# Kernel tuning notes

Hardware: AMD Instinct MI355X
Metric: run time of the kernel (lower is better)

The kernel has to match this reference:

```python
import jax, jax.numpy as jnp
import numpy as np

BATCH = 16384
NFEAT = 16          # 12 non-rainfall + 4 rainfall (indices 12..15)
NNON, NRAIN = 12, 4
NC = 1000           # n_clusters
DM = 64             # d_model
DI = 128            # d_inner = expand * d_model
DS = 16             # d_state
DC = 4              # d_conv
DR = 4              # dt_rank = ceil(d_model / 16)
NL = 4              # n_layers
EPS = 1e-5


def _silu(v):
    return v * jax.nn.sigmoid(v)


def _layernorm(v, g, b):
    m = jnp.mean(v, -1, keepdims=True)
    s = jnp.mean(jnp.square(v - m), -1, keepdims=True)
    return (v - m) * jax.lax.rsqrt(s + EPS) * g + b


def _mamba(x, ipw, cw, cb, xpw, dtw, dtb, alog, dskip, opw):
    # x: [B, L, DM]
    Bsz, L, _ = x.shape
    xz = x @ ipw                                # [B, L, 2*DI]
    xc, z = jnp.split(xz, 2, axis=-1)
    # causal depthwise conv1d (kernel DC, left pad DC-1)
    xp = jnp.pad(xc, ((0, 0), (DC - 1, 0), (0, 0)))
    xc = sum(xp[:, k:k + L, :] * cw[:, k] for k in range(DC)) + cb
    xc = _silu(xc)
    proj = xc @ xpw                             # [B, L, DR + 2*DS]
    dt = jax.nn.softplus(proj[..., :DR] @ dtw + dtb)   # [B, L, DI]
    Bm = proj[..., DR:DR + DS]                  # [B, L, DS]
    Cm = proj[..., DR + DS:]                    # [B, L, DS]
    A = -jnp.exp(alog)                          # [DI, DS]
    dA = jnp.exp(dt[..., None] * A)             # [B, L, DI, DS]
    dBx = dt[..., None] * Bm[:, :, None, :] * xc[..., None]

    def step(h, ab):
        a, b = ab
        h = a * h + b
        return h, h

    _, hs = jax.lax.scan(step, jnp.zeros((Bsz, DI, DS), x.dtype),
                         (jnp.swapaxes(dA, 0, 1), jnp.swapaxes(dBx, 0, 1)))
    hs = jnp.swapaxes(hs, 0, 1)                 # [B, L, DI, DS]
    y = jnp.einsum('blds,bls->bld', hs, Cm) + dskip * xc
    y = y * _silu(z)
    return y @ opw                              # [B, L, DM]


def _branch(feat, w_in, b_in, ipw, cw, cb, xpw, dtw, dtb, alog, dskip, opw, ln_g, ln_b):
    x = (feat @ w_in + b_in)[:, None, :]        # [B, 1, DM]
    for l in range(NL):
        x = x + _layernorm(
            _mamba(x, ipw[l], cw[l], cb[l], xpw[l], dtw[l], dtb[l], alog[l], dskip[l], opw[l]),
            ln_g[l], ln_b[l])
    return jnp.mean(x, axis=1)                  # [B, DM]


def _forward(x, w_nr, b_nr, w_r, b_r, w_in_nr, b_in_nr, w_in_r, b_in_r,
             ipw, cw, cb, xpw, dtw, dtb, alog, dskip, opw, ln_g, ln_b,
             head_w1, head_b1, head_w2, head_b2):
    nr = x[:, :NNON] @ w_nr + b_nr              # non-rainfall cluster proj [B, NC]
    r = x[:, NNON:] @ w_r + b_r                 # rainfall cluster proj [B, NC]
    # NOTE: mamba layers + norms are SHARED between both branches (as in the torch module)
    o_nr = _branch(nr, w_in_nr, b_in_nr, ipw, cw, cb, xpw, dtw, dtb, alog, dskip, opw, ln_g, ln_b)
    o_r = _branch(r, w_in_r, b_in_r, ipw, cw, cb, xpw, dtw, dtb, alog, dskip, opw, ln_g, ln_b)
    h = jnp.concatenate([o_nr, o_r], axis=-1)   # [B, 2*DM]
    h = jax.nn.relu(h @ head_w1 + head_b1)
    return (h @ head_w2 + head_b2)[:, 0]        # [B]


def setup_inputs() -> dict:
    key = jax.random.key(0)
    kit = iter(jax.random.split(key, 32))

    def rn(shape, s=0.05):
        return jax.random.normal(next(kit), shape, jnp.float32) * s

    return {
        'x': jax.random.normal(next(kit), (BATCH, NFEAT), jnp.float32),
        'w_nr': rn((NNON, NC)), 'b_nr': rn((NC,)),
        'w_r': rn((NRAIN, NC)), 'b_r': rn((NC,)),
        'w_in_nr': rn((NC, DM)), 'b_in_nr': rn((DM,)),
        'w_in_r': rn((NC, DM)), 'b_in_r': rn((DM,)),
        'ipw': rn((NL, DM, 2 * DI)),
        'cw': rn((NL, DI, DC)), 'cb': rn((NL, DI)),
        'xpw': rn((NL, DI, DR + 2 * DS)),
        'dtw': rn((NL, DR, DI)), 'dtb': rn((NL, DI)),
        'alog': jnp.log(jnp.broadcast_to(jnp.arange(1, DS + 1, dtype=jnp.float32), (NL, DI, DS))),
        'dskip': jnp.ones((NL, DI), jnp.float32),
        'opw': rn((NL, DI, DM)),
        'ln_g': jnp.ones((NL, DM), jnp.float32),
        'ln_b': jnp.zeros((NL, DM), jnp.float32),
        'head_w1': rn((2 * DM, 32)), 'head_b1': rn((32,)),
        'head_w2': rn((32, 1)), 'head_b2': rn((1,)),
    }


def reference(x, w_nr, b_nr, w_r, b_r, w_in_nr, b_in_nr, w_in_r, b_in_r,
              ipw, cw, cb, xpw, dtw, dtb, alog, dskip, opw, ln_g, ln_b,
              head_w1, head_b1, head_w2, head_b2):
    return _forward(x, w_nr, b_nr, w_r, b_r, w_in_nr, b_in_nr, w_in_r, b_in_r,
                    ipw, cw, cb, xpw, dtw, dtb, alog, dskip, opw, ln_g, ln_b,
                    head_w1, head_b1, head_w2, head_b2)
```

## Files before the change

### kernel.cpp

```cpp
#include <hip/hip_runtime.h>
#include <hip/hip_bf16.h>
#include <math.h>

typedef unsigned short u16;
typedef unsigned int u32;
typedef __attribute__((ext_vector_type(8))) short bf8v;
typedef __attribute__((ext_vector_type(4))) float f32x4;

#define BR   32
#define LR   64
#define NLAY 4

#define U_IPH 4096
#define U_IPL (U_IPH + 65536)
#define U_XPH (U_IPL + 65536)
#define U_XPL (U_XPH + 24576)
#define U_OPH (U_XPL + 24576)
#define U_OPL (U_OPH + 32768)

__device__ __forceinline__ float b2f(u16 u) {
  u32 x = ((u32)u) << 16; return __uint_as_float(x);
}
__device__ __forceinline__ u16 f2b(float f) {
  __hip_bfloat16 b = __float2bfloat16(f);
  return __builtin_bit_cast(u16, b);
}
__device__ __forceinline__ void splitbf(float v, u16& h, u16& l) {
  h = f2b(v);
  l = f2b(v - b2f(h));
}
__device__ __forceinline__ float siluf(float v) { return v / (1.f + __expf(-v)); }
__device__ __forceinline__ float softplusf(float v) {
  return fmaxf(v, 0.f) + __logf(1.f + __expf(-fabsf(v)));
}
__device__ __forceinline__ int sxIdx(int r, int c) {
  return r * 64 + ((((c >> 3) ^ r) & 7) << 3) + (c & 7);
}
__device__ __forceinline__ int szIdx(int r, int c) {
  int ch = c >> 3;
  int chs = (ch & 8) | ((ch ^ r) & 7);
  return r * 128 + chs * 8 + (c & 7);
}

#define MFMA16(A, B, C) __builtin_amdgcn_mfma_f32_16x16x32_bf16(A, B, C, 0, 0, 0)

extern "C" __global__ __launch_bounds__(256)
void prep_all_kernel(const float* __restrict__ w_nr, const float* __restrict__ b_nr,
                     const float* __restrict__ w_r,  const float* __restrict__ b_r,
                     const float* __restrict__ win_nr, const float* __restrict__ bin_nr,
                     const float* __restrict__ win_r,  const float* __restrict__ bin_r,
                     const float* __restrict__ ipw, const float* __restrict__ xpw,
                     const float* __restrict__ opw,
                     float* __restrict__ wsf, u16* __restrict__ wsu) {
  __shared__ float snr[1000];
  __shared__ float sr_[1000];
  const int bid = blockIdx.x, tid = threadIdx.x;
  if (bid < 64) {
    const int j = bid;
    for (int k = tid; k < 1000; k += 256) {
      snr[k] = win_nr[(size_t)k * 64 + j];
      sr_[k] = win_r [(size_t)k * 64 + j];
    }
    __syncthreads();
    const int grp = tid >> 4;
    const int ks  = tid & 15;
    const int k0 = ks * 63, k1 = (k0 + 63 < 1000) ? k0 + 63 : 1000;
    for (int o = grp; o < 18; o += 16) {
      float acc = 0.f;
      if (o < 12) {
        const float* s = w_nr + (size_t)o * 1000;
        for (int k = k0; k < k1; ++k) acc = fmaf(s[k], snr[k], acc);
      } else if (o == 12) {
        for (int k = k0; k < k1; ++k) acc = fmaf(b_nr[k], snr[k], acc);
      } else if (o < 17) {
        const float* s = w_r + (size_t)(o - 13) * 1000;
        for (int k = k0; k < k1; ++k) acc = fmaf(s[k], sr_[k], acc);
      } else {
        for (int k = k0; k < k1; ++k) acc = fmaf(b_r[k], sr_[k], acc);
      }
      for (int off = 1; off < 16; off <<= 1) acc += __shfl_xor(acc, off, 64);
      if (ks == 0) {
        if (o < 12)       wsf[o * 64 + j] = acc;
        else if (o == 12) wsf[768 + j]  = acc + bin_nr[j];
        else if (o < 17)  wsf[832 + (o - 13) * 64 + j] = acc;
        else              wsf[1088 + j] = acc + bin_r[j];
      }
    }
    return;
  }
  int gid = (bid - 64) * 256 + tid;
  float v; int dh, dl;
  if (gid < 65536) {
    int l = gid >> 14, rem = gid & 16383;
    int n = rem & 255, k = rem >> 8;
    v = ipw[(size_t)l * 16384 + k * 256 + n];
    int o = l * 16384 + n * 64 + k;
    dh = U_IPH + o; dl = U_IPL + o;
  } else if (gid < 65536 + 18432) {
    int e = gid - 65536;
    int l = e / 4608, r2 = e - l * 4608;
    int k = r2 / 36, n = r2 - k * 36;
    v = xpw[(size_t)l * 4608 + k * 36 + n];
    int o = l * 6144 + n * 128 + k;
    dh = U_XPH + o; dl = U_XPL + o;
  } else if (gid < 65536 + 18432 + 6144) {
    int e = gid - 83968;
    int l = e / 1536, r3 = e - l * 1536;
    int n = 36 + (r3 >> 7), k = r3 & 127;
    v = 0.f;
    int o = l * 6144 + n * 128 + k;
    dh = U_XPH + o; dl = U_XPL + o;
  } else {
    int e = gid - 90112;
    int l = e >> 13, rem = e & 8191;
    int n = rem & 63, k = rem >> 6;
    v = opw[(size_t)l * 8192 + k * 64 + n];
    int o = l * 8192 + n * 128 + k;
    dh = U_OPH + o; dl = U_OPL + o;
  }
  u16 h, lo; splitbf(v, h, lo);
  wsu[dh] = h; wsu[dl] = lo;
}

extern "C" __global__ __launch_bounds__(512, 3)
void mamba_main_kernel(const float* __restrict__ xin, const float* __restrict__ wsf,
                       const u16* __restrict__ wsu,
                       const float* __restrict__ cw, const float* __restrict__ cbi,
                       const float* __restrict__ dtw, const float* __restrict__ dtb,
                       const float* __restrict__ dskip,
                       const float* __restrict__ lng, const float* __restrict__ lnb,
                       const float* __restrict__ hw1, const float* __restrict__ hb1,
                       const float* __restrict__ hw2, const float* __restrict__ hb2,
                       float* __restrict__ outp)
{
  __shared__ __align__(16) u16 sxh[LR * 64], sxl[LR * 64];
  __shared__ __align__(16) u16 szh[LR * 128], szl[LR * 128];
  __shared__ __align__(16) u16 szb[LR * 128];
  __shared__ __align__(16) float sproj[LR * 48];
  __shared__ float spart[4][LR][2];
  __shared__ float sbc[LR];

  const int tid = threadIdx.x;
  const int wv = tid >> 6, lane = tid & 63;
  const int col16 = lane & 15, g = lane >> 4;
  const int r0 = blockIdx.x * BR;

  for (int idx = tid; idx < LR * 64; idx += 512) {
    int r = idx >> 6, c = idx & 63;
    const float* xr = xin + (size_t)(r0 + (r & 31)) * 16;
    float acc;
    if (r < 32) {
      acc = wsf[768 + c];
      #pragma unroll
      for (int i = 0; i < 12; ++i) acc = fmaf(xr[i], wsf[i * 64 + c], acc);
    } else {
      acc = wsf[1088 + c];
      #pragma unroll
      for (int i = 0; i < 4; ++i) acc = fmaf(xr[12 + i], wsf[832 + i * 64 + c], acc);
    }
    u16 h, lo; splitbf(acc, h, lo);
    int di = sxIdx(r, c); sxh[di] = h; sxl[di] = lo;
  }

  for (int l = 0; l < NLAY; ++l) {
    __syncthreads();
    {
      const u16* iph = wsu + U_IPH + l * 16384;
      const u16* ipl_ = wsu + U_IPL + l * 16384;
      const bool isZ = (wv >= 4);
      #pragma unroll 1
      for (int tt = 0; tt < 2; ++tt) {
        const int tile = 2 * wv + tt;
        const int n = tile * 16 + col16;
        bf8v Wh0 = *(const bf8v*)&iph[n * 64 + g * 8];
        bf8v Wl0 = *(const bf8v*)&ipl_[n * 64 + g * 8];
        bf8v Wh1 = *(const bf8v*)&iph[n * 64 + 32 + g * 8];
        bf8v Wl1 = *(const bf8v*)&ipl_[n * 64 + 32 + g * 8];
        float c3 = 0.f, cc = 0.f;
        int colx = (tile & 7) * 16 + col16;
        if (!isZ) {
          c3 = cw[(size_t)l * 512 + colx * 4 + 3];
          cc = cbi[(size_t)l * 128 + colx];
        }
        #pragma unroll 1
        for (int rt = 0; rt < 4; ++rt) {
          const int rowA = rt * 16 + col16;
          bf8v Ah0 = *(const bf8v*)&sxh[rowA * 64 + (((g ^ rowA) & 7) << 3)];
          bf8v Al0 = *(const bf8v*)&sxl[rowA * 64 + (((g ^ rowA) & 7) << 3)];
          bf8v Ah1 = *(const bf8v*)&sxh[rowA * 64 + ((((4 + g) ^ rowA) & 7) << 3)];
          bf8v Al1 = *(const bf8v*)&sxl[rowA * 64 + ((((4 + g) ^ rowA) & 7) << 3)];
          f32x4 acc = {0, 0, 0, 0};
          acc = MFMA16(Ah0, Wh0, acc);
          acc = MFMA16(Al0, Wh0, acc);
          acc = MFMA16(Ah0, Wl0, acc);
          acc = MFMA16(Ah1, Wh1, acc);
          acc = MFMA16(Al1, Wh1, acc);
          acc = MFMA16(Ah1, Wl1, acc);
          #pragma unroll
          for (int j = 0; j < 4; ++j) {
            int row = rt * 16 + g * 4 + j;
            if (!isZ) {
              float v = siluf(fmaf(acc[j], c3, cc));
              u16 h, lo; splitbf(v, h, lo);
              int di = szIdx(row, colx);
              szh[di] = h; szl[di] = lo;
            } else {
              szb[szIdx(row, colx)] = f2b(siluf(acc[j]));
            }
          }
        }
      }
    }
    __syncthreads();
    {
      const u16* xph = wsu + U_XPH + l * 6144;
      const u16* xpl = wsu + U_XPL + l * 6144;
      const int rt = wv & 3;
      const int rowA = rt * 16 + col16;
      const int ntasks = (wv < 4) ? 2 : 1;
      #pragma unroll 1
      for (int q = 0; q < ntasks; ++q) {
        const int nt = (wv < 4) ? q : 2;
        const int n2 = nt * 16 + col16;
        f32x4 C = {0, 0, 0, 0};
        #pragma unroll
        for (int ks = 0; ks < 4; ++ks) {
          int ch = ks * 4 + g;
          int ai = rowA * 128 + (((ch & 8) | ((ch ^ rowA) & 7)) << 3);
          bf8v Ah = *(const bf8v*)&szh[ai];
          bf8v Al = *(const bf8v*)&szl[ai];
          bf8v Wh = *(const bf8v*)&xph[n2 * 128 + ks * 32 + g * 8];
          bf8v Wl = *(const bf8v*)&xpl[n2 * 128 + ks * 32 + g * 8];
          C = MFMA16(Ah, Wh, C);
          C = MFMA16(Al, Wh, C);
          C = MFMA16(Ah, Wl, C);
        }
        #pragma unroll
        for (int j = 0; j < 4; ++j)
          sproj[(rt * 16 + g * 4 + j) * 48 + nt * 16 + col16] = C[j];
      }
    }
    __syncthreads();
    {
      int r = tid >> 3, s = tid & 7;
      float v = sproj[r * 48 + 4 + s] * sproj[r * 48 + 20 + s]
              + sproj[r * 48 + 12 + s] * sproj[r * 48 + 28 + s];
      v += __shfl_xor(v, 1); v += __shfl_xor(v, 2); v += __shfl_xor(v, 4);
      if (s == 0) sbc[r] = v;
    }
    __syncthreads();
    {
      const int rt = wv & 3;
      const int ctb = (wv >> 2) * 4;
      #pragma unroll 1
      for (int t = 0; t < 4; ++t) {
        int col = (ctb + t) * 16 + col16;
        float w0 = dtw[(size_t)l * 512 + col];
        float w1 = dtw[(size_t)l * 512 + 128 + col];
        float w2 = dtw[(size_t)l * 512 + 256 + col];
        float w3 = dtw[(size_t)l * 512 + 384 + col];
        float bb = dtb[(size_t)l * 128 + col];
        float ds = dskip[(size_t)l * 128 + col];
        #pragma unroll
        for (int j = 0; j < 4; ++j) {
          int r = rt * 16 + g * 4 + j;
          float4 pj = *(const float4*)&sproj[r * 48];
          float dtv = softplusf(fmaf(pj.w, w3, fmaf(pj.z, w2, fmaf(pj.y, w1, fmaf(pj.x, w0, bb)))));
          int di = szIdx(r, col);
          float xc = b2f(szh[di]) + b2f(szl[di]);
          float zv = b2f(szb[di]);
          float y = xc * fmaf(dtv, sbc[r], ds) * zv;
          u16 h, lo; splitbf(y, h, lo);
          szh[di] = h; szl[di] = lo;
        }
      }
    }
    __syncthreads();
    f32x4 O0 = {0,0,0,0}, O1 = {0,0,0,0};
    {
      const u16* oph = wsu + U_OPH + l * 8192;
      const u16* opl = wsu + U_OPL + l * 8192;
      const int nt = wv & 3, rtp = wv >> 2;
      const int n = nt * 16 + col16;
      #pragma unroll
      for (int ks = 0; ks < 4; ++ks) {
        bf8v Wh = *(const bf8v*)&oph[n * 128 + ks * 32 + g * 8];
        bf8v Wl = *(const bf8v*)&opl[n * 128 + ks * 32 + g * 8];
        int ch = ks * 4 + g;
        #pragma unroll
        for (int rr = 0; rr < 2; ++rr) {
          int rowA = (2 * rtp + rr) * 16 + col16;
          int ai = rowA * 128 + (((ch & 8) | ((ch ^ rowA) & 7)) << 3);
          bf8v Ah = *(const bf8v*)&szh[ai];
          bf8v Al = *(const bf8v*)&szl[ai];
          if (rr == 0) {
            O0 = MFMA16(Ah, Wh, O0); O0 = MFMA16(Al, Wh, O0); O0 = MFMA16(Ah, Wl, O0);
          } else {
            O1 = MFMA16(Ah, Wh, O1); O1 = MFMA16(Al, Wh, O1); O1 = MFMA16(Ah, Wl, O1);
          }
        }
      }
      #pragma unroll
      for (int rr = 0; rr < 2; ++rr) {
        #pragma unroll
        for (int j = 0; j < 4; ++j) {
          float o = (rr == 0) ? O0[j] : O1[j];
          float s1 = o, s2 = o * o;
          s1 += __shfl_xor(s1, 1); s2 += __shfl_xor(s2, 1);
          s1 += __shfl_xor(s1, 2); s2 += __shfl_xor(s2, 2);
          s1 += __shfl_xor(s1, 4); s2 += __shfl_xor(s2, 4);
          s1 += __shfl_xor(s1, 8); s2 += __shfl_xor(s2, 8);
          if (col16 == 0) {
            int row = (2 * rtp + rr) * 16 + g * 4 + j;
            spart[nt][row][0] = s1; spart[nt][row][1] = s2;
          }
        }
      }
    }
    __syncthreads();
    {
      const int nt = wv & 3, rtp = wv >> 2;
      int col = nt * 16 + col16;
      float gv = lng[(size_t)l * 64 + col], bv = lnb[(size_t)l * 64 + col];
      #pragma unroll
      for (int rr = 0; rr < 2; ++rr) {
        #pragma unroll
        for (int j = 0; j < 4; ++j) {
          int row = (2 * rtp + rr) * 16 + g * 4 + j;
          float s1 = spart[0][row][0] + spart[1][row][0] + spart[2][row][0] + spart[3][row][0];
          float s2 = spart[0][row][1] + spart[1][row][1] + spart[2][row][1] + spart[3][row][1];
          float m = s1 * (1.f / 64);
          float var = s2 * (1.f / 64) - m * m;
          float rstd = rsqrtf(var + 1e-5f);
          float o = (rr == 0) ? O0[j] : O1[j];
          float v = fmaf((o - m) * rstd, gv, bv);
          int di = sxIdx(row, col);
          float nv = b2f(sxh[di]) + b2f(sxl[di]) + v;
          u16 h, lo; splitbf(nv, h, lo);
          sxh[di] = h; sxl[di] = lo;
        }
      }
    }
  }
  __syncthreads();
  {
    int k = tid >> 2, n0 = (tid & 3) * 8;
    const float* src = hw1 + (size_t)k * 32 + n0;
    #pragma unroll
    for (int i = 0; i < 8; ++i) {
      u16 h, lo; splitbf(src[i], h, lo);
      int di = szIdx(n0 + i, k);
      szh[di] = h; szl[di] = lo;
    }
  }
  __syncthreads();
  if (wv < 4) {
    const int mt = wv & 1, nt = wv >> 1;
    const int m16 = mt * 16 + col16;
    const int nB = nt * 16 + col16;
    f32x4 H = {0, 0, 0, 0};
    #pragma unroll
    for (int ks = 0; ks < 4; ++ks) {
      int kg = ks * 32 + g * 8;
      int arow = m16 + ((kg >> 6) << 5);
      int ai = sxIdx(arow, kg & 63);
      bf8v Ah = *(const bf8v*)&sxh[ai];
      bf8v Al = *(const bf8v*)&sxl[ai];
      int bi = szIdx(nB, kg);
      bf8v Bh = *(const bf8v*)&szh[bi];
      bf8v Bl = *(const bf8v*)&szl[bi];
      H = MFMA16(Ah, Bh, H);
      H = MFMA16(Al, Bh, H);
      H = MFMA16(Ah, Bl, H);
    }
    float bias = hb1[nB];
    #pragma unroll
    for (int j = 0; j < 4; ++j) {
      int m = mt * 16 + g * 4 + j;
      sproj[m * 48 + nB] = fmaxf(H[j] + bias, 0.f);
    }
  }
  __syncthreads();
  if (tid < 256) {
    int m = tid >> 3, s = tid & 7;
    float acc = sproj[m * 48 + s] * hw2[s]
              + sproj[m * 48 + 8 + s] * hw2[8 + s]
              + sproj[m * 48 + 16 + s] * hw2[16 + s]
              + sproj[m * 48 + 24 + s] * hw2[24 + s];
    acc += __shfl_xor(acc, 1); acc += __shfl_xor(acc, 2); acc += __shfl_xor(acc, 4);
    if (s == 0) outp[r0 + m] = acc + hb2[0];
  }
}

extern "C" void kernel_launch(void* const* d_in, const int* in_sizes, int n_in,
                              void* d_out, int out_size, void* d_ws, size_t ws_size,
                              hipStream_t stream) {
  const float* x      = (const float*)d_in[0];
  const float* w_nr   = (const float*)d_in[1];
  const float* b_nr   = (const float*)d_in[2];
  const float* w_r    = (const float*)d_in[3];
  const float* b_r    = (const float*)d_in[4];
  const float* win_nr = (const float*)d_in[5];
  const float* bin_nr = (const float*)d_in[6];
  const float* win_r  = (const float*)d_in[7];
  const float* bin_r  = (const float*)d_in[8];
  const float* ipw    = (const float*)d_in[9];
  const float* cw     = (const float*)d_in[10];
  const float* cb     = (const float*)d_in[11];
  const float* xpw    = (const float*)d_in[12];
  const float* dtw    = (const float*)d_in[13];
  const float* dtb    = (const float*)d_in[14];
  const float* dskip  = (const float*)d_in[16];
  const float* opw    = (const float*)d_in[17];
  const float* lng    = (const float*)d_in[18];
  const float* lnb    = (const float*)d_in[19];
  const float* hw1    = (const float*)d_in[20];
  const float* hb1    = (const float*)d_in[21];
  const float* hw2    = (const float*)d_in[22];
  const float* hb2    = (const float*)d_in[23];
  float* wsf = (float*)d_ws;
  u16*   wsu = (u16*)d_ws;
  float* out = (float*)d_out;

  prep_all_kernel<<<544, 256, 0, stream>>>(w_nr, b_nr, w_r, b_r,
                                           win_nr, bin_nr, win_r, bin_r,
                                           ipw, xpw, opw, wsf, wsu);
  mamba_main_kernel<<<16384 / BR, 512, 0, stream>>>(x, wsf, wsu, cw, cb,
                                                    dtw, dtb, dskip, lng, lnb,
                                                    hw1, hb1, hw2, hb2, out);
}
```

Measured before the change: 225.2 us.

## Restructure weight-prep kernel with LDS-tiled transposes and vectorized bf16 split stores

Rewrites the prep kernel that folds the cluster projections and converts the Mamba weights to split bf16. The fold now uses one block per output row, reading win coalesced across lanes. The weight transposes stage tiles in padded shared memory and write the hi/lo parts as 16-byte vectors instead of scattered 2-byte stores. The grid shrinks from 544 to 42 blocks, so each block does more serial work and fewer CUs are used for a small prologue.

```diff
diff --git a/kernel.cpp b/kernel.cpp
--- a/kernel.cpp
+++ b/kernel.cpp
@@ -52,74 +52,110 @@
                      const float* __restrict__ ipw, const float* __restrict__ xpw,
                      const float* __restrict__ opw,
                      float* __restrict__ wsf, u16* __restrict__ wsu) {
-  __shared__ float snr[1000];
-  __shared__ float sr_[1000];
+  __shared__ float tileF[128 * 65];
   const int bid = blockIdx.x, tid = threadIdx.x;
-  if (bid < 64) {
-    const int j = bid;
-    for (int k = tid; k < 1000; k += 256) {
-      snr[k] = win_nr[(size_t)k * 64 + j];
-      sr_[k] = win_r [(size_t)k * 64 + j];
-    }
-    __syncthreads();
-    const int grp = tid >> 4;
-    const int ks  = tid & 15;
-    const int k0 = ks * 63, k1 = (k0 + 63 < 1000) ? k0 + 63 : 1000;
-    for (int o = grp; o < 18; o += 16) {
-      float acc = 0.f;
-      if (o < 12) {
-        const float* s = w_nr + (size_t)o * 1000;
-        for (int k = k0; k < k1; ++k) acc = fmaf(s[k], snr[k], acc);
-      } else if (o == 12) {
-        for (int k = k0; k < k1; ++k) acc = fmaf(b_nr[k], snr[k], acc);
-      } else if (o < 17) {
-        const float* s = w_r + (size_t)(o - 13) * 1000;
-        for (int k = k0; k < k1; ++k) acc = fmaf(s[k], sr_[k], acc);
-      } else {
-        for (int k = k0; k < k1; ++k) acc = fmaf(b_r[k], sr_[k], acc);
-      }
-      for (int off = 1; off < 16; off <<= 1) acc += __shfl_xor(acc, off, 64);
-      if (ks == 0) {
-        if (o < 12)       wsf[o * 64 + j] = acc;
-        else if (o == 12) wsf[768 + j]  = acc + bin_nr[j];
-        else if (o < 17)  wsf[832 + (o - 13) * 64 + j] = acc;
-        else              wsf[1088 + j] = acc + bin_r[j];
-      }
+  const int lane = tid & 63, wv4 = tid >> 6;
+
+  if (bid < 18) {
+    const int o = bid;
+    const float* win = (o < 13) ? win_nr : win_r;
+    const float* wr;
+    if (o < 12)       wr = w_nr + (size_t)o * 1000;
+    else if (o == 12) wr = b_nr;
+    else if (o < 17)  wr = w_r + (size_t)(o - 13) * 1000;
+    else              wr = b_r;
+    float acc = 0.f;
+    const int k0 = wv4 * 250, k1 = k0 + 250;
+    for (int k = k0; k < k1; ++k)
+      acc = fmaf(wr[k], win[(size_t)k * 64 + lane], acc);
+    tileF[wv4 * 64 + lane] = acc;
+    __syncthreads();
+    if (tid < 64) {
+      float v = tileF[tid] + tileF[64 + tid] + tileF[128 + tid] + tileF[192 + tid];
+      if (o < 12)       wsf[o * 64 + tid] = v;
+      else if (o == 12) wsf[768 + tid]  = v + bin_nr[tid];
+      else if (o < 17)  wsf[832 + (o - 13) * 64 + tid] = v;
+      else              wsf[1088 + tid] = v + bin_r[tid];
     }
     return;
   }
-  int gid = (bid - 64) * 256 + tid;
-  float v; int dh, dl;
-  if (gid < 65536) {
-    int l = gid >> 14, rem = gid & 16383;
-    int n = rem & 255, k = rem >> 8;
-    v = ipw[(size_t)l * 16384 + k * 256 + n];
-    int o = l * 16384 + n * 64 + k;
-    dh = U_IPH + o; dl = U_IPL + o;
-  } else if (gid < 65536 + 18432) {
-    int e = gid - 65536;
-    int l = e / 4608, r2 = e - l * 4608;
-    int k = r2 / 36, n = r2 - k * 36;
-    v = xpw[(size_t)l * 4608 + k * 36 + n];
-    int o = l * 6144 + n * 128 + k;
-    dh = U_XPH + o; dl = U_XPL + o;
-  } else if (gid < 65536 + 18432 + 6144) {
-    int e = gid - 83968;
-    int l = e / 1536, r3 = e - l * 1536;
-    int n = 36 + (r3 >> 7), k = r3 & 127;
-    v = 0.f;
-    int o = l * 6144 + n * 128 + k;
-    dh = U_XPH + o; dl = U_XPL + o;
-  } else {
-    int e = gid - 90112;
-    int l = e >> 13, rem = e & 8191;
-    int n = rem & 63, k = rem >> 6;
-    v = opw[(size_t)l * 8192 + k * 64 + n];
-    int o = l * 8192 + n * 128 + k;
-    dh = U_OPH + o; dl = U_OPL + o;
-  }
-  u16 h, lo; splitbf(v, h, lo);
-  wsu[dh] = h; wsu[dl] = lo;
+
+  if (bid < 34) {
+    const int t = bid - 18;
+    const int l = t >> 2, n0 = (t & 3) * 64;
+    #pragma unroll
+    for (int rr = 0; rr < 16; ++rr) {
+      int k = rr * 4 + wv4;
+      tileF[k * 65 + lane] = ipw[(size_t)l * 16384 + k * 256 + n0 + lane];
+    }
+    __syncthreads();
+    const int n = tid >> 2, kc = tid & 3;
+    size_t o = (size_t)l * 16384 + (n0 + n) * 64 + kc * 16;
+    #pragma unroll
+    for (int c = 0; c < 2; ++c) {
+      bf8v hv, lv;
+      #pragma unroll
+      for (int i = 0; i < 8; ++i) {
+        int k = kc * 16 + c * 8 + i;
+        u16 h, lo; splitbf(tileF[k * 65 + n], h, lo);
+        hv[i] = (short)h; lv[i] = (short)lo;
+      }
+      *(bf8v*)&wsu[U_IPH + o + c * 8] = hv;
+      *(bf8v*)&wsu[U_IPL + o + c * 8] = lv;
+    }
+    return;
+  }
+
+  if (bid < 38) {
+    const int l = bid - 34;
+    for (int idx = tid; idx < 4608; idx += 256) {
+      int k = idx / 36, n = idx - k * 36;
+      tileF[k * 37 + n] = xpw[(size_t)l * 4608 + idx];
+    }
+    __syncthreads();
+    if (tid < 192) {
+      const int n = tid >> 2, kc = tid & 3;
+      size_t o = (size_t)l * 6144 + n * 128 + kc * 32;
+      #pragma unroll
+      for (int c = 0; c < 4; ++c) {
+        bf8v hv, lv;
+        #pragma unroll
+        for (int i = 0; i < 8; ++i) {
+          int k = kc * 32 + c * 8 + i;
+          float v = (n < 36) ? tileF[k * 37 + n] : 0.f;
+          u16 h, lo; splitbf(v, h, lo);
+          hv[i] = (short)h; lv[i] = (short)lo;
+        }
+        *(bf8v*)&wsu[U_XPH + o + c * 8] = hv;
+        *(bf8v*)&wsu[U_XPL + o + c * 8] = lv;
+      }
+    }
+    return;
+  }
+
+  {
+    const int l = bid - 38;
+    #pragma unroll
+    for (int rr = 0; rr < 32; ++rr) {
+      int k = rr * 4 + wv4;
+      tileF[k * 65 + lane] = opw[(size_t)l * 8192 + k * 64 + lane];
+    }
+    __syncthreads();
+    const int n = tid >> 2, kc = tid & 3;
+    size_t o = (size_t)l * 8192 + n * 128 + kc * 32;
+    #pragma unroll
+    for (int c = 0; c < 4; ++c) {
+      bf8v hv, lv;
+      #pragma unroll
+      for (int i = 0; i < 8; ++i) {
+        int k = kc * 32 + c * 8 + i;
+        u16 h, lo; splitbf(tileF[k * 65 + n], h, lo);
+        hv[i] = (short)h; lv[i] = (short)lo;
+      }
+      *(bf8v*)&wsu[U_OPH + o + c * 8] = hv;
+      *(bf8v*)&wsu[U_OPL + o + c * 8] = lv;
+    }
+  }
 }
 
 extern "C" __global__ __launch_bounds__(512, 3)
@@ -422,9 +458,9 @@
   u16*   wsu = (u16*)d_ws;
   float* out = (float*)d_out;
 
-  prep_all_kernel<<<544, 256, 0, stream>>>(w_nr, b_nr, w_r, b_r,
-                                           win_nr, bin_nr, win_r, bin_r,
-                                           ipw, xpw, opw, wsf, wsu);
+  prep_all_kernel<<<42, 256, 0, stream>>>(w_nr, b_nr, w_r, b_r,
+                                          win_nr, bin_nr, win_r, bin_r,
+                                          ipw, xpw, opw, wsf, wsu);
   mamba_main_kernel<<<16384 / BR, 512, 0, stream>>>(x, wsf, wsu, cw, cb,
                                                     dtw, dtb, dskip, lng, lnb,
                                                     hw1, hb1, hw2, hb2, out);
```

After: 206.8 us. 8.2% less time.
